# Kernel tuning notes

Measured on AMD Instinct MI355X. Metric: run time of the kernel, lower is better.

Reference implementation:

```python
import jax, jax.numpy as jnp
import numpy as np

B, H, V, T = 2048, 512, 64, 128

def setup_inputs() -> dict:
    key = jax.random.key(0)
    ks = jax.random.split(key, 7)
    s = 1.0 / np.sqrt(H)
    return {
        "z": jax.random.normal(ks[0], (B, H), dtype=jnp.float32),
        "w_ih": jax.random.uniform(ks[1], (4 * H, H), jnp.float32, -s, s),
        "w_hh": jax.random.uniform(ks[2], (4 * H, H), jnp.float32, -s, s),
        "b_ih": jax.random.uniform(ks[3], (4 * H,), jnp.float32, -s, s),
        "b_hh": jax.random.uniform(ks[4], (4 * H,), jnp.float32, -s, s),
        "fc_w": jax.random.uniform(ks[5], (V, H), jnp.float32, -s, s),
        "fc_b": jax.random.uniform(ks[6], (V,), jnp.float32, -s, s),
    }

def reference(z, w_ih, w_hh, b_ih, b_hh, fc_w, fc_b):
    batch = z.shape[0]
    # Input z is identical at every timestep -> precompute its gate contribution once.
    x_gates = z @ w_ih.T + b_ih + b_hh  # [B, 4H]

    def step(carry, _):
        h, c = carry
        gates = x_gates + h @ w_hh.T  # [B, 4H]
        i, f, g, o = jnp.split(gates, 4, axis=-1)  # PyTorch LSTMCell gate order
        i = jax.nn.sigmoid(i)
        f = jax.nn.sigmoid(f)
        g = jnp.tanh(g)
        o = jax.nn.sigmoid(o)
        c = f * c + i * g
        h = o * jnp.tanh(c)
        return (h, c), h

    h0 = jnp.zeros((batch, w_hh.shape[1]), dtype=z.dtype)
    c0 = jnp.zeros_like(h0)
    _, hs = jax.lax.scan(step, (h0, c0), None, length=T)  # [T, B, H]
    x = jnp.transpose(hs, (1, 0, 2))  # [B, T, H]
    return jax.nn.relu(x @ fc_w.T + fc_b)  # [B, T, V]
```

## Files before the change

kernel.cpp:

```cpp
#include <hip/hip_runtime.h>
#include <hip/hip_bf16.h>
#include <cstdint>

#define B_   2048
#define H_   512
#define T_   128
#define V_   64
#define FOURH 2048

typedef __bf16 bf16x8 __attribute__((ext_vector_type(8)));
typedef float  floatx4 __attribute__((ext_vector_type(4)));
typedef int    intx4   __attribute__((ext_vector_type(4)));

__device__ __forceinline__ unsigned short f2bf(float f) {
    union { float f; uint32_t u; } v; v.f = f;
    uint32_t r = v.u + 0x7fff + ((v.u >> 16) & 1);
    return (unsigned short)(r >> 16);
}

__device__ __forceinline__ float rcp_(float x) {
    float r; asm("v_rcp_f32 %0, %1" : "=v"(r) : "v"(x)); return r;
}
__device__ __forceinline__ float sigmoidf_(float x) {
    return rcp_(1.0f + __expf(-x));
}
__device__ __forceinline__ float tanhf_(float x) {
    float e = __expf(fminf(-2.0f * x, 80.0f));
    return (1.0f - e) * rcp_(1.0f + e);
}

__device__ __forceinline__ void global_to_lds16(const unsigned short* g, unsigned short* l) {
    __builtin_amdgcn_global_load_lds(
        (const __attribute__((address_space(1))) unsigned int*)g,
        (__attribute__((address_space(3))) unsigned int*)l, 16, 0, 0);
}

__device__ __forceinline__ bf16x8 load16_sys(const unsigned short* p) {
    bf16x8 d;
    asm volatile("global_load_dwordx4 %0, %1, off sc0 sc1\n\t"
                 "s_waitcnt vmcnt(0)"
                 : "=v"(d) : "v"(p));
    return d;
}

__device__ __forceinline__ void flag_prefetch(const unsigned int* fp, intx4& f) {
    asm volatile("global_load_dwordx4 %0, %1, off sc0 sc1"
                 : "=v"(f) : "v"(fp) : "memory");
}
__device__ __forceinline__ bool flag_ok(const intx4& f, unsigned int tgt) {
    return (unsigned int)f[0] >= tgt && (unsigned int)f[1] >= tgt &&
           (unsigned int)f[2] >= tgt && (unsigned int)f[3] >= tgt;
}
__device__ __forceinline__ void wait4(const unsigned int* fp, unsigned int tgt) {
    for (;;) {
        intx4 f;
        asm volatile("global_load_dwordx4 %0, %1, off sc0 sc1\n\t"
                     "s_waitcnt vmcnt(0)" : "=v"(f) : "v"(fp) : "memory");
        if (flag_ok(f, tgt)) return;
        __builtin_amdgcn_s_sleep(1);
    }
}
__device__ __forceinline__ void flag_post(unsigned int* p, unsigned int v) {
    asm volatile("global_store_dword %0, %1, off sc0 sc1" :: "v"(p), "v"(v) : "memory");
}

__global__ void prep_kernel(const float* __restrict__ z,
                            const float* __restrict__ w_ih,
                            const float* __restrict__ w_hh,
                            const float* __restrict__ b_ih,
                            const float* __restrict__ b_hh,
                            const float* __restrict__ fc_w,
                            unsigned short* __restrict__ Bp_ih,
                            unsigned short* __restrict__ Bp_hh,
                            unsigned short* __restrict__ z_bf,
                            unsigned short* __restrict__ fcw_bf,
                            float* __restrict__ biasp,
                            unsigned int* __restrict__ cnt) {
    int i = blockIdx.x * blockDim.x + threadIdx.x;
    int col = i >> 9, k = i & 511;
    int jj = col >> 7, cc = col & 127;
    int gate = (cc >> 4) & 3;
    int hcl = ((cc >> 6) << 4) | (cc & 15);
    int p = gate * 512 + jj * 32 + hcl;
    Bp_hh[i] = f2bf(w_hh[p * 512 + k]);
    Bp_ih[i] = f2bf(w_ih[p * 512 + k]);
    z_bf[i]  = f2bf(z[i]);
    if (i < V_ * H_) fcw_bf[i] = f2bf(fc_w[i]);
    if (i < FOURH) {
        int j2 = i >> 7, c2 = i & 127;
        int g2 = (c2 >> 4) & 3;
        int h2 = ((c2 >> 6) << 4) | (c2 & 15);
        int p2 = g2 * 512 + j2 * 32 + h2;
        biasp[i] = b_ih[p2] + b_hh[p2];
    }
    if (i < 2048) cnt[i] = 0;
}

__device__ __forceinline__ void gemm_tile_r1(
        const unsigned short* __restrict__ Aglob,
        const unsigned short* __restrict__ Bglob,
        int arow0, int brow0,
        unsigned short* As, unsigned short* Bs,
        floatx4 acc[2][8], int w, int l) {
    const int lr = l >> 3;
    const int gl = (l & 7) ^ lr;
    const int ln = l & 15, lq = l >> 4, ls = l & 7;
    for (int kc = 0; kc < 8; ++kc) {
        const int kof = kc * 64 + gl * 8;
        #pragma unroll
        for (int q = 0; q < 4; ++q) {
            const int r0 = (w * 4 + q) * 8;
            global_to_lds16(Aglob + (size_t)(arow0 + r0 + lr) * 512 + kof, As + r0 * 64);
            global_to_lds16(Bglob + (size_t)(brow0 + r0 + lr) * 512 + kof, Bs + r0 * 64);
        }
        __syncthreads();
        #pragma unroll
        for (int kk = 0; kk < 2; ++kk) {
            bf16x8 a[2], b[8];
            #pragma unroll
            for (int mt = 0; mt < 2; ++mt) {
                const int m = 32 * w + 16 * mt + ln;
                const int g = kk * 4 + lq;
                a[mt] = *(const bf16x8*)(As + m * 64 + ((g ^ ls) * 8));
            }
            #pragma unroll
            for (int nt = 0; nt < 8; ++nt) {
                const int n = 16 * nt + ln;
                const int g = kk * 4 + lq;
                b[nt] = *(const bf16x8*)(Bs + n * 64 + ((g ^ ls) * 8));
            }
            #pragma unroll
            for (int mt = 0; mt < 2; ++mt)
                #pragma unroll
                for (int nt = 0; nt < 8; ++nt)
                    acc[mt][nt] = __builtin_amdgcn_mfma_f32_16x16x32_bf16(
                        a[mt], b[nt], acc[mt][nt], 0, 0, 0);
        }
        __syncthreads();
    }
}

__global__ void __launch_bounds__(256) xg_gemm_kernel(
        const unsigned short* __restrict__ z_bf,
        const unsigned short* __restrict__ Bp_ih,
        const float* __restrict__ biasp,
        float* __restrict__ xg) {
    __shared__ unsigned short As[128 * 64];
    __shared__ unsigned short Bs[128 * 64];
    const int bi = blockIdx.x, j = blockIdx.y;
    const int tid = threadIdx.x, w = tid >> 6, l = tid & 63;
    floatx4 acc[2][8];
    const floatx4 zf = {0.f, 0.f, 0.f, 0.f};
    for (int a1 = 0; a1 < 2; ++a1) for (int a2 = 0; a2 < 8; ++a2) acc[a1][a2] = zf;

    gemm_tile_r1(z_bf, Bp_ih, bi * 128, j * 128, As, Bs, acc, w, l);

    const int ln = l & 15, lq = l >> 4;
    #pragma unroll
    for (int mt = 0; mt < 2; ++mt)
        #pragma unroll
        for (int nt = 0; nt < 8; ++nt) {
            const int colp = j * 128 + nt * 16 + ln;
            const float bv = biasp[colp];
            #pragma unroll
            for (int r = 0; r < 4; ++r) {
                const int b = bi * 128 + 32 * w + 16 * mt + lq * 4 + r;
                xg[(size_t)b * FOURH + colp] = acc[mt][nt][r] + bv;
            }
        }
}

__device__ __forceinline__ void stage_issue2(const unsigned short* __restrict__ Aglob,
                                             int arow0, int kc, int w, int l,
                                             intx4& t0, intx4& t1) {
    const int lr = l >> 3;
    const int gl = (l & 7) ^ lr;
    const int kof = kc * 64 + gl * 8;
    const unsigned short* p0 = Aglob + (size_t)(arow0 + (w * 2 + 0) * 8 + lr) * 512 + kof;
    const unsigned short* p1 = Aglob + (size_t)(arow0 + (w * 2 + 1) * 8 + lr) * 512 + kof;
    asm volatile(
        "global_load_dwordx4 %0, %2, off sc0 sc1\n\t"
        "global_load_dwordx4 %1, %3, off sc0 sc1"
        : "=&v"(t0), "=&v"(t1)
        : "v"(p0), "v"(p1)
        : "memory");
}

template<int N>
__device__ __forceinline__ void commit4c(unsigned short* buf, int w, int l,
                                         const intx4* u) {
    if constexpr (N == 12) asm volatile("s_waitcnt vmcnt(12)" ::: "memory");
    else if constexpr (N == 8)  asm volatile("s_waitcnt vmcnt(8)"  ::: "memory");
    else if constexpr (N == 4)  asm volatile("s_waitcnt vmcnt(4)"  ::: "memory");
    else                        asm volatile("s_waitcnt vmcnt(0)"  ::: "memory");
    const int lr = l >> 3, sl = (l & 7) * 8;
    #pragma unroll
    for (int kcL = 0; kcL < 2; ++kcL)
        #pragma unroll
        for (int q = 0; q < 2; ++q)
            *(intx4*)(buf + kcL * 4096 + ((w * 2 + q) * 8 + lr) * 64 + sl) = u[kcL * 2 + q];
}

__global__ void __launch_bounds__(256, 1) lstm_persistent(
        const unsigned short* __restrict__ Bp_hh,
        const unsigned short* __restrict__ fcw_bf,
        const float* __restrict__ xg,
        const float* __restrict__ fc_b,
        unsigned short* __restrict__ h0b,
        unsigned short* __restrict__ h1b,
        unsigned int* __restrict__ cnt,
        float* __restrict__ out) {
    __shared__ unsigned short AsB0[4096 * 2];
    __shared__ unsigned short AsB1[4096 * 2];

    const int bx = blockIdx.x;
    const int gi = bx & 31;
    const int j  = bx >> 5;
    const int tid = threadIdx.x;
    const int w = tid >> 6, l = tid & 63;
    const int ln = l & 15, lq = l >> 4;
    const bool jlt4 = (j < 4);
    const int j16 = j * 16;
    const int v = 16 * w + ln;
    const float fcb_v = fc_b[v];
    const int arow0 = gi * 64;
    const int colbase = j * 256 + (w >> 1) * 128 + (w & 1) * 64;
    unsigned int* flagp = cnt + gi * 64;
    const floatx4 zf = {0.f, 0.f, 0.f, 0.f};

    bf16x8 bq[16][4];
    {
        const unsigned short* bbase =
            Bp_hh + ((size_t)(colbase + ln)) * 512 + lq * 8;
        #pragma unroll
        for (int s = 0; s < 16; ++s)
            #pragma unroll
            for (int nt = 0; nt < 4; ++nt)
                bq[s][nt] = *(const bf16x8*)(bbase + (size_t)nt * 16 * 512 + s * 32);
    }

    floatx4 xga[4][4];
    #pragma unroll
    for (int mt = 0; mt < 4; ++mt)
        #pragma unroll
        for (int nt = 0; nt < 4; ++nt)
            #pragma unroll
            for (int r = 0; r < 4; ++r) {
                const int b = arow0 + 16 * mt + lq * 4 + r;
                xga[mt][nt][r] = xg[(size_t)b * FOURH + colbase + 16 * nt + ln];
            }

    unsigned short* hlds = AsB0;

    float cst[4][4];
    #pragma unroll
    for (int mt = 0; mt < 4; ++mt)
        #pragma unroll
        for (int r = 0; r < 4; ++r) {
            float iv = sigmoidf_(xga[mt][0][r]);
            float gv = tanhf_  (xga[mt][2][r]);
            float ov = sigmoidf_(xga[mt][3][r]);
            float cv = iv * gv;
            cst[mt][r] = cv;
            hlds[(16 * mt + lq * 4 + r) * 64 + (16 * w + ln)] = f2bf(ov * tanhf_(cv));
        }
    __syncthreads();
    for (int c = tid; c < 512; c += 256) {
        const int row = c >> 3, seg = c & 7;
        intx4 d = *(const intx4*)(hlds + row * 64 + seg * 8);
        const unsigned short* p = h0b + (size_t)(arow0 + row) * 512 + j * 64 + seg * 8;
        asm volatile("global_store_dwordx4 %0, %1, off sc0 sc1" :: "v"(p), "v"(d) : "memory");
    }
    asm volatile("s_waitcnt vmcnt(0)" ::: "memory");
    __syncthreads();
    if (tid == 0) flag_post(flagp + j, 1u);
    intx4 fpreA, fpreB;
    flag_prefetch(flagp,     fpreA);
    flag_prefetch(flagp + 4, fpreB);

    unsigned short* hb[2] = {h0b, h1b};
    #pragma unroll 1
    for (int t = 1; t < T_; ++t) {
        const unsigned int tg = (unsigned int)t;

        asm volatile("s_waitcnt vmcnt(0)" ::: "memory");
        __builtin_amdgcn_sched_barrier(0);
        if (!(flag_ok(fpreA, tg) && flag_ok(fpreB, tg))) {
            wait4(flagp, tg);
            wait4(flagp + 4, tg);
        }

        const unsigned short* hprev = hb[(t - 1) & 1];
        unsigned short* hnext = hb[t & 1];

        floatx4 acc[4][4];
        #pragma unroll
        for (int a1 = 0; a1 < 4; ++a1)
            #pragma unroll
            for (int a2 = 0; a2 < 4; ++a2) acc[a1][a2] = zf;
        floatx4 pacc = zf;

        intx4 u[16];
        #pragma unroll
        for (int g = 0; g < 4; ++g) {
            stage_issue2(hprev, arow0, 2 * g,     w, l, u[4 * g + 0], u[4 * g + 1]);
            stage_issue2(hprev, arow0, 2 * g + 1, w, l, u[4 * g + 2], u[4 * g + 3]);
        }
        commit4c<12>(AsB0, w, l, &u[0]);
        __syncthreads();

        #pragma unroll
        for (int g = 0; g < 4; ++g) {
            const unsigned short* buf = (g & 1) ? AsB1 : AsB0;
            #pragma unroll
            for (int ss = 0; ss < 4; ++ss) {
                const int s = g * 4 + ss;
                const int ga = (ss & 1) * 4 + lq;
                const unsigned short* Ac = buf + (ss >> 1) * 4096;
                bf16x8 af[4];
                #pragma unroll
                for (int mt = 0; mt < 4; ++mt) {
                    const int m = 16 * mt + ln;
                    af[mt] = *(const bf16x8*)(Ac + m * 64 + ((ga ^ (ln & 7)) * 8));
                }
                #pragma unroll
                for (int mt = 0; mt < 4; ++mt)
                    #pragma unroll
                    for (int nt = 0; nt < 4; ++nt)
                        acc[mt][nt] = __builtin_amdgcn_mfma_f32_16x16x32_bf16(
                            af[mt], bq[s][nt], acc[mt][nt], 0, 0, 0);
                if (jlt4) {
                    bf16x8 ap = *(const bf16x8*)(Ac + (j16 + ln) * 64 + ((ga ^ (ln & 7)) * 8));
                    bf16x8 bp = *(const bf16x8*)(fcw_bf + (size_t)v * 512 + s * 32 + lq * 8);
                    pacc = __builtin_amdgcn_mfma_f32_16x16x32_bf16(ap, bp, pacc, 0, 0, 0);
                }
            }
            if (g == 0) { commit4c<8>(AsB1, w, l, &u[4]);  __syncthreads(); }
            else if (g == 1) { commit4c<4>(AsB0, w, l, &u[8]);  __syncthreads(); }
            else if (g == 2) { commit4c<0>(AsB1, w, l, &u[12]); __syncthreads(); }
        }

        #pragma unroll
        for (int mt = 0; mt < 4; ++mt)
            #pragma unroll
            for (int r = 0; r < 4; ++r) {
                float iv = sigmoidf_(acc[mt][0][r] + xga[mt][0][r]);
                float fv = sigmoidf_(acc[mt][1][r] + xga[mt][1][r]);
                float gv = tanhf_  (acc[mt][2][r] + xga[mt][2][r]);
                float ov = sigmoidf_(acc[mt][3][r] + xga[mt][3][r]);
                float cn = fv * cst[mt][r] + iv * gv;
                cst[mt][r] = cn;
                hlds[(16 * mt + lq * 4 + r) * 64 + (16 * w + ln)] = f2bf(ov * tanhf_(cn));
            }
        __syncthreads();
        for (int c = tid; c < 512; c += 256) {
            const int row = c >> 3, seg = c & 7;
            intx4 d = *(const intx4*)(hlds + row * 64 + seg * 8);
            const unsigned short* p = hnext + (size_t)(arow0 + row) * 512 + j * 64 + seg * 8;
            asm volatile("global_store_dwordx4 %0, %1, off sc0 sc1" :: "v"(p), "v"(d) : "memory");
        }
        asm volatile("s_waitcnt vmcnt(0)" ::: "memory");
        __syncthreads();
        if (tid == 0) flag_post(flagp + j, tg + 1u);
        flag_prefetch(flagp,     fpreA);
        flag_prefetch(flagp + 4, fpreB);

        if (jlt4) {
            #pragma unroll
            for (int r = 0; r < 4; ++r) {
                const int b = arow0 + j16 + lq * 4 + r;
                out[(size_t)b * (T_ * V_) + (t - 1) * V_ + v] = fmaxf(pacc[r] + fcb_v, 0.0f);
            }
        }
    }

    if (jlt4) {
        wait4(flagp,     T_);
        wait4(flagp + 4, T_);
        const unsigned short* hlast = hb[(T_ - 1) & 1];
        floatx4 pa = zf;
        const int ar = arow0 + j16 + ln;
        #pragma unroll
        for (int kc = 0; kc < 16; ++kc) {
            const int k = kc * 32 + lq * 8;
            bf16x8 a = load16_sys(hlast + (size_t)ar * 512 + k);
            bf16x8 b = *(const bf16x8*)(fcw_bf + (size_t)v * 512 + k);
            pa = __builtin_amdgcn_mfma_f32_16x16x32_bf16(a, b, pa, 0, 0, 0);
        }
        #pragma unroll
        for (int r = 0; r < 4; ++r) {
            const int b = arow0 + j16 + lq * 4 + r;
            out[(size_t)b * (T_ * V_) + (T_ - 1) * V_ + v] = fmaxf(pa[r] + fcb_v, 0.0f);
        }
    }
}

extern "C" void kernel_launch(void* const* d_in, const int* in_sizes, int n_in,
                              void* d_out, int out_size, void* d_ws, size_t ws_size,
                              hipStream_t stream) {
    const float* z    = (const float*)d_in[0];
    const float* w_ih = (const float*)d_in[1];
    const float* w_hh = (const float*)d_in[2];
    const float* b_ih = (const float*)d_in[3];
    const float* b_hh = (const float*)d_in[4];
    const float* fc_w = (const float*)d_in[5];
    const float* fc_b = (const float*)d_in[6];
    float* out = (float*)d_out;

    char* ws = (char*)d_ws;
    size_t o = 0;
    auto take = [&](size_t bytes) { char* p = ws + o; o += (bytes + 255) & ~(size_t)255; return p; };
    unsigned short* Bp_hh  = (unsigned short*)take((size_t)FOURH * H_ * 2);
    unsigned short* Bp_ih  = (unsigned short*)take((size_t)FOURH * H_ * 2);
    unsigned short* z_bf   = (unsigned short*)take((size_t)B_ * H_ * 2);
    unsigned short* fcw_bf = (unsigned short*)take((size_t)V_ * H_ * 2);
    float*          biasp  = (float*)take((size_t)FOURH * 4);
    unsigned short* hbuf0  = (unsigned short*)take((size_t)B_ * H_ * 2);
    unsigned short* hbuf1  = (unsigned short*)take((size_t)B_ * H_ * 2);
    unsigned int*   cnt    = (unsigned int*)take(32 * 256);
    float*          xg     = (float*)take((size_t)B_ * FOURH * 4);

    prep_kernel<<<(B_ * H_) / 256, 256, 0, stream>>>(z, w_ih, w_hh, b_ih, b_hh, fc_w,
                                                     Bp_ih, Bp_hh, z_bf, fcw_bf, biasp, cnt);
    xg_gemm_kernel<<<dim3(16, 16), 256, 0, stream>>>(z_bf, Bp_ih, biasp, xg);
    lstm_persistent<<<256, 256, 0, stream>>>(Bp_hh, fcw_bf, xg, fc_b,
                                             hbuf0, hbuf1, cnt, out);
}
```

Before: 1.525 ms.

## Replace per-step flag barriers with poisoned-sentinel ring buffer for hidden state

Drops the per-timestep flag post and poll between the cooperating blocks. Hidden state now goes into a 16-deep ring of buffers. Each stripe is pre-filled with a bf16 sentinel (0xFF80, negative infinity), and consumers re-load any chunk that still holds the sentinel until real data arrives. Loads for the next step are issued right after the current stores, and each chunk is checked on its own, so the wait overlaps with the MFMA work. The scheme relies on bf16 h values never equalling the sentinel, uses 16x the hidden-state memory, and adds poison stores that run ahead of readers.

```diff
diff --git a/kernel.cpp b/kernel.cpp
--- a/kernel.cpp
+++ b/kernel.cpp
@@ -7,6 +7,7 @@
 #define T_   128
 #define V_   64
 #define FOURH 2048
+#define NBUF 16
 
 typedef __bf16 bf16x8 __attribute__((ext_vector_type(8)));
 typedef float  floatx4 __attribute__((ext_vector_type(4)));
@@ -43,10 +44,6 @@
     return d;
 }
 
-__device__ __forceinline__ void flag_prefetch(const unsigned int* fp, intx4& f) {
-    asm volatile("global_load_dwordx4 %0, %1, off sc0 sc1"
-                 : "=v"(f) : "v"(fp) : "memory");
-}
 __device__ __forceinline__ bool flag_ok(const intx4& f, unsigned int tgt) {
     return (unsigned int)f[0] >= tgt && (unsigned int)f[1] >= tgt &&
            (unsigned int)f[2] >= tgt && (unsigned int)f[3] >= tgt;
@@ -62,6 +59,16 @@
 }
 __device__ __forceinline__ void flag_post(unsigned int* p, unsigned int v) {
     asm volatile("global_store_dword %0, %1, off sc0 sc1" :: "v"(p), "v"(v) : "memory");
+}
+
+__device__ __forceinline__ bool stale16(const intx4& r) {
+    bool s = false;
+    #pragma unroll
+    for (int k = 0; k < 4; ++k) {
+        unsigned int d = (unsigned int)r[k];
+        s = s || ((d & 0xFFFFu) == 0xFF80u) || ((d >> 16) == 0xFF80u);
+    }
+    return s;
 }
 
 __global__ void prep_kernel(const float* __restrict__ z,
@@ -75,6 +82,7 @@
                             unsigned short* __restrict__ z_bf,
                             unsigned short* __restrict__ fcw_bf,
                             float* __restrict__ biasp,
+                            unsigned short* __restrict__ hring,
                             unsigned int* __restrict__ cnt) {
     int i = blockIdx.x * blockDim.x + threadIdx.x;
     int col = i >> 9, k = i & 511;
@@ -94,6 +102,13 @@
         biasp[i] = b_ih[p2] + b_hh[p2];
     }
     if (i < 2048) cnt[i] = 0;
+    {
+        intx4* hp = (intx4*)hring;
+        const intx4 pz = {(int)0xFF80FF80u, (int)0xFF80FF80u,
+                          (int)0xFF80FF80u, (int)0xFF80FF80u};
+        hp[i] = pz;
+        hp[i + (1 << 20)] = pz;
+    }
 }
 
 __device__ __forceinline__ void gemm_tile_r1(
@@ -186,19 +201,31 @@
         : "memory");
 }
 
-template<int N>
-__device__ __forceinline__ void commit4c(unsigned short* buf, int w, int l,
-                                         const intx4* u) {
-    if constexpr (N == 12) asm volatile("s_waitcnt vmcnt(12)" ::: "memory");
-    else if constexpr (N == 8)  asm volatile("s_waitcnt vmcnt(8)"  ::: "memory");
-    else if constexpr (N == 4)  asm volatile("s_waitcnt vmcnt(4)"  ::: "memory");
-    else                        asm volatile("s_waitcnt vmcnt(0)"  ::: "memory");
+__device__ __forceinline__ void issue_chunk(const unsigned short* __restrict__ hprev,
+                                            int arow0, int g, int w, int l, intx4* u4) {
+    stage_issue2(hprev, arow0, 2 * g,     w, l, u4[0], u4[1]);
+    stage_issue2(hprev, arow0, 2 * g + 1, w, l, u4[2], u4[3]);
+}
+
+__device__ __forceinline__ void commit4(unsigned short* buf, int w, int l,
+                                        const intx4* u) {
     const int lr = l >> 3, sl = (l & 7) * 8;
     #pragma unroll
     for (int kcL = 0; kcL < 2; ++kcL)
         #pragma unroll
         for (int q = 0; q < 2; ++q)
             *(intx4*)(buf + kcL * 4096 + ((w * 2 + q) * 8 + lr) * 64 + sl) = u[kcL * 2 + q];
+}
+
+__device__ __forceinline__ void poison_stripe(unsigned short* __restrict__ buf,
+                                              int arow0, int j, int tid) {
+    const intx4 pz = {(int)0xFF80FF80u, (int)0xFF80FF80u,
+                      (int)0xFF80FF80u, (int)0xFF80FF80u};
+    for (int c = tid; c < 512; c += 256) {
+        const int row = c >> 3, seg = c & 7;
+        const unsigned short* p = buf + (size_t)(arow0 + row) * 512 + j * 64 + seg * 8;
+        asm volatile("global_store_dwordx4 %0, %1, off sc0 sc1" :: "v"(p), "v"(pz) : "memory");
+    }
 }
 
 __global__ void __launch_bounds__(256, 1) lstm_persistent(
@@ -206,8 +233,7 @@
         const unsigned short* __restrict__ fcw_bf,
         const float* __restrict__ xg,
         const float* __restrict__ fc_b,
-        unsigned short* __restrict__ h0b,
-        unsigned short* __restrict__ h1b,
+        unsigned short* __restrict__ hring,
         unsigned int* __restrict__ cnt,
         float* __restrict__ out) {
     __shared__ unsigned short AsB0[4096 * 2];
@@ -228,6 +254,10 @@
     unsigned int* flagp = cnt + gi * 64;
     const floatx4 zf = {0.f, 0.f, 0.f, 0.f};
 
+    auto hbuf = [&](int t) -> unsigned short* {
+        return hring + ((size_t)(t & (NBUF - 1)) << 20);
+    };
+
     bf16x8 bq[16][4];
     {
         const unsigned short* bbase =
@@ -268,30 +298,19 @@
     for (int c = tid; c < 512; c += 256) {
         const int row = c >> 3, seg = c & 7;
         intx4 d = *(const intx4*)(hlds + row * 64 + seg * 8);
-        const unsigned short* p = h0b + (size_t)(arow0 + row) * 512 + j * 64 + seg * 8;
+        const unsigned short* p = hbuf(0) + (size_t)(arow0 + row) * 512 + j * 64 + seg * 8;
         asm volatile("global_store_dwordx4 %0, %1, off sc0 sc1" :: "v"(p), "v"(d) : "memory");
     }
-    asm volatile("s_waitcnt vmcnt(0)" ::: "memory");
     __syncthreads();
-    if (tid == 0) flag_post(flagp + j, 1u);
-    intx4 fpreA, fpreB;
-    flag_prefetch(flagp,     fpreA);
-    flag_prefetch(flagp + 4, fpreB);
-
-    unsigned short* hb[2] = {h0b, h1b};
+
+    intx4 u[16];
+    poison_stripe(hbuf(9), arow0, j, tid);
+    #pragma unroll
+    for (int g = 0; g < 4; ++g) issue_chunk(hbuf(0), arow0, g, w, l, &u[4 * g]);
+
     #pragma unroll 1
     for (int t = 1; t < T_; ++t) {
-        const unsigned int tg = (unsigned int)t;
-
-        asm volatile("s_waitcnt vmcnt(0)" ::: "memory");
-        __builtin_amdgcn_sched_barrier(0);
-        if (!(flag_ok(fpreA, tg) && flag_ok(fpreB, tg))) {
-            wait4(flagp, tg);
-            wait4(flagp + 4, tg);
-        }
-
-        const unsigned short* hprev = hb[(t - 1) & 1];
-        unsigned short* hnext = hb[t & 1];
+        const unsigned short* hprev = hbuf(t - 1);
 
         floatx4 acc[4][4];
         #pragma unroll
@@ -300,18 +319,29 @@
             for (int a2 = 0; a2 < 4; ++a2) acc[a1][a2] = zf;
         floatx4 pacc = zf;
 
-        intx4 u[16];
         #pragma unroll
         for (int g = 0; g < 4; ++g) {
-            stage_issue2(hprev, arow0, 2 * g,     w, l, u[4 * g + 0], u[4 * g + 1]);
-            stage_issue2(hprev, arow0, 2 * g + 1, w, l, u[4 * g + 2], u[4 * g + 3]);
-        }
-        commit4c<12>(AsB0, w, l, &u[0]);
-        __syncthreads();
-
-        #pragma unroll
-        for (int g = 0; g < 4; ++g) {
-            const unsigned short* buf = (g & 1) ? AsB1 : AsB0;
+            if (g == 0)      asm volatile("s_waitcnt vmcnt(12)" ::: "memory");
+            else if (g == 1) asm volatile("s_waitcnt vmcnt(8)"  ::: "memory");
+            else if (g == 2) asm volatile("s_waitcnt vmcnt(4)"  ::: "memory");
+            else             asm volatile("s_waitcnt vmcnt(0)"  ::: "memory");
+            __builtin_amdgcn_sched_barrier(0);
+
+            bool st = stale16(u[4 * g + 0]) || stale16(u[4 * g + 1]) ||
+                      stale16(u[4 * g + 2]) || stale16(u[4 * g + 3]);
+            while (__any((int)st)) {
+                __builtin_amdgcn_s_sleep(1);
+                issue_chunk(hprev, arow0, g, w, l, &u[4 * g]);
+                asm volatile("s_waitcnt vmcnt(0)" ::: "memory");
+                __builtin_amdgcn_sched_barrier(0);
+                st = stale16(u[4 * g + 0]) || stale16(u[4 * g + 1]) ||
+                     stale16(u[4 * g + 2]) || stale16(u[4 * g + 3]);
+            }
+
+            unsigned short* buf = (g & 1) ? AsB1 : AsB0;
+            commit4(buf, w, l, &u[4 * g]);
+            __syncthreads();
+
             #pragma unroll
             for (int ss = 0; ss < 4; ++ss) {
                 const int s = g * 4 + ss;
@@ -335,9 +365,6 @@
                     pacc = __builtin_amdgcn_mfma_f32_16x16x32_bf16(ap, bp, pacc, 0, 0, 0);
                 }
             }
-            if (g == 0) { commit4c<8>(AsB1, w, l, &u[4]);  __syncthreads(); }
-            else if (g == 1) { commit4c<4>(AsB0, w, l, &u[8]);  __syncthreads(); }
-            else if (g == 2) { commit4c<0>(AsB1, w, l, &u[12]); __syncthreads(); }
         }
 
         #pragma unroll
@@ -353,17 +380,16 @@
                 hlds[(16 * mt + lq * 4 + r) * 64 + (16 * w + ln)] = f2bf(ov * tanhf_(cn));
             }
         __syncthreads();
-        for (int c = tid; c < 512; c += 256) {
-            const int row = c >> 3, seg = c & 7;
-            intx4 d = *(const intx4*)(hlds + row * 64 + seg * 8);
-            const unsigned short* p = hnext + (size_t)(arow0 + row) * 512 + j * 64 + seg * 8;
-            asm volatile("global_store_dwordx4 %0, %1, off sc0 sc1" :: "v"(p), "v"(d) : "memory");
-        }
-        asm volatile("s_waitcnt vmcnt(0)" ::: "memory");
+        {
+            unsigned short* hnext = hbuf(t);
+            for (int c = tid; c < 512; c += 256) {
+                const int row = c >> 3, seg = c & 7;
+                intx4 d = *(const intx4*)(hlds + row * 64 + seg * 8);
+                const unsigned short* p = hnext + (size_t)(arow0 + row) * 512 + j * 64 + seg * 8;
+                asm volatile("global_store_dwordx4 %0, %1, off sc0 sc1" :: "v"(p), "v"(d) : "memory");
+            }
+        }
         __syncthreads();
-        if (tid == 0) flag_post(flagp + j, tg + 1u);
-        flag_prefetch(flagp,     fpreA);
-        flag_prefetch(flagp + 4, fpreB);
 
         if (jlt4) {
             #pragma unroll
@@ -372,12 +398,22 @@
                 out[(size_t)b * (T_ * V_) + (t - 1) * V_ + v] = fmaxf(pacc[r] + fcb_v, 0.0f);
             }
         }
+
+        if (t < T_ - 1) {
+            poison_stripe(hbuf(t + 9), arow0, j, tid);
+            #pragma unroll
+            for (int g = 0; g < 4; ++g) issue_chunk(hbuf(t), arow0, g, w, l, &u[4 * g]);
+        } else {
+            asm volatile("s_waitcnt vmcnt(0)" ::: "memory");
+            __syncthreads();
+            if (tid == 0) flag_post(flagp + j, 1u);
+        }
     }
 
     if (jlt4) {
-        wait4(flagp,     T_);
-        wait4(flagp + 4, T_);
-        const unsigned short* hlast = hb[(T_ - 1) & 1];
+        wait4(flagp,     1u);
+        wait4(flagp + 4, 1u);
+        const unsigned short* hlast = hbuf(T_ - 1);
         floatx4 pa = zf;
         const int ar = arow0 + j16 + ln;
         #pragma unroll
@@ -415,14 +451,14 @@
     unsigned short* z_bf   = (unsigned short*)take((size_t)B_ * H_ * 2);
     unsigned short* fcw_bf = (unsigned short*)take((size_t)V_ * H_ * 2);
     float*          biasp  = (float*)take((size_t)FOURH * 4);
-    unsigned short* hbuf0  = (unsigned short*)take((size_t)B_ * H_ * 2);
-    unsigned short* hbuf1  = (unsigned short*)take((size_t)B_ * H_ * 2);
     unsigned int*   cnt    = (unsigned int*)take(32 * 256);
+    unsigned short* hring  = (unsigned short*)take((size_t)NBUF * B_ * H_ * 2);
     float*          xg     = (float*)take((size_t)B_ * FOURH * 4);
 
     prep_kernel<<<(B_ * H_) / 256, 256, 0, stream>>>(z, w_ih, w_hh, b_ih, b_hh, fc_w,
-                                                     Bp_ih, Bp_hh, z_bf, fcw_bf, biasp, cnt);
+                                                     Bp_ih, Bp_hh, z_bf, fcw_bf, biasp,
+                                                     hring, cnt);
     xg_gemm_kernel<<<dim3(16, 16), 256, 0, stream>>>(z_bf, Bp_ih, biasp, xg);
     lstm_persistent<<<256, 256, 0, stream>>>(Bp_hh, fcw_bf, xg, fc_b,
-                                             hbuf0, hbuf1, cnt, out);
-}
+                                             hring, cnt, out);
+}
```

Measured after the change: 2.110 ms. +38.4%, slower.
